# Performance work log

Measured on AMD Instinct MI355X. Metric: run time of the kernel, lower is better.

Reference implementation:

```python
import jax, jax.numpy as jnp
import numpy as np

B, T, H = 65536, 34, 64
T10_LO, T10_HI = 0.1, 5.0
M0_LO, M0_HI = 0.0, 10000.0


def setup_inputs() -> dict:
    key = jax.random.key(0)
    ks = jax.random.split(key, 24)
    sig = jax.random.uniform(ks[0], (B, T), jnp.float32, 0.1, 1.0)
    keep = jax.random.uniform(ks[1], (B, T)) > 0.3
    X_fa_in = jnp.where(keep, sig, 0.0)
    fa_vals = jax.random.uniform(ks[2], (B, T), jnp.float32, 0.05, 0.6)  # flip angles (rad)
    fa_mask = keep
    fa_len = jnp.sum(keep, axis=1).astype(jnp.int64)
    TR_vals = jax.random.uniform(ks[3], (B, 1), jnp.float32, 0.003, 0.01)
    gi = 1.0 / np.sqrt(H)
    p = {}
    p['gru_Wih'] = jax.random.uniform(ks[4], (3 * H, 2), jnp.float32, -gi, gi)
    p['gru_Whh'] = jax.random.uniform(ks[5], (3 * H, H), jnp.float32, -gi, gi)
    p['gru_bih'] = jax.random.uniform(ks[6], (3 * H,), jnp.float32, -gi, gi)
    p['gru_bhh'] = jax.random.uniform(ks[7], (3 * H,), jnp.float32, -gi, gi)
    p['score_T10_w'] = jax.random.normal(ks[8], (H,), jnp.float32) * gi
    p['score_M0_w'] = jax.random.normal(ks[9], (H,), jnp.float32) * gi
    def lin(kw, kb, fan_out, fan_in):
        b = 1.0 / np.sqrt(fan_in)
        return (jax.random.uniform(kw, (fan_out, fan_in), jnp.float32, -b, b),
                jax.random.uniform(kb, (fan_out,), jnp.float32, -b, b))
    p['regT_W1'], p['regT_b1'] = lin(ks[10], ks[11], 200, H)
    p['regT_W2'], p['regT_b2'] = lin(ks[12], ks[13], 200, 200)
    p['regT_W3'], p['regT_b3'] = lin(ks[14], ks[15], 1, 200)
    p['regM_W1'], p['regM_b1'] = lin(ks[16], ks[17], 200, H)
    p['regM_W2'], p['regM_b2'] = lin(ks[18], ks[19], 200, 200)
    p['regM_W3'], p['regM_b3'] = lin(ks[20], ks[21], 1, 200)
    return dict(X_fa_in=X_fa_in, fa_vals=fa_vals, fa_mask=fa_mask, fa_len=fa_len,
                TR_vals=TR_vals, **p)


def _forward_fill(X_fa_in, fa_vals):
    # Segmented last-observation-carried-forward via cummax of valid indices.
    valid = X_fa_in != 0
    idx = jnp.where(valid, jnp.arange(T)[None, :], -1)
    last = jax.lax.cummax(idx, axis=1)                     # [B,T] index of last nonzero
    g = jnp.clip(last, 0, T - 1)
    Xf = jnp.where(last >= 0, jnp.take_along_axis(X_fa_in, g, axis=1), 0.0)
    ff = jnp.where(last >= 0, jnp.take_along_axis(fa_vals, g, axis=1), 0.0)
    return Xf, ff


def _gru(x, Wih, Whh, bih, bhh):
    # x: [B,T,2] -> out: [B,T,H]; PyTorch GRU gate order (r, z, n)
    x_proj = jnp.einsum('btf,gf->btg', x, Wih) + bih       # [B,T,3H]
    def step(h, xp):
        gh = h @ Whh.T + bhh                               # [B,3H]
        xr, xz, xn = jnp.split(xp, 3, axis=-1)
        hr, hz, hn = jnp.split(gh, 3, axis=-1)
        r = jax.nn.sigmoid(xr + hr)
        z = jax.nn.sigmoid(xz + hz)
        n = jnp.tanh(xn + r * hn)
        h_new = (1.0 - z) * n + z * h
        return h_new, h_new
    h0 = jnp.zeros((x.shape[0], Whh.shape[1]), x.dtype)
    _, out = jax.lax.scan(step, h0, jnp.swapaxes(x_proj, 0, 1))
    return jnp.swapaxes(out, 0, 1)


def _mlp(h, W1, b1, W2, b2, W3, b3):
    # Dropout layers are identity in eval mode
    h = jax.nn.elu(h @ W1.T + b1)
    h = jax.nn.elu(h @ W2.T + b2)
    return h @ W3.T + b3


def reference(X_fa_in, fa_vals, fa_mask, fa_len, TR_vals,
              gru_Wih, gru_Whh, gru_bih, gru_bhh,
              score_T10_w, score_M0_w,
              regT_W1, regT_b1, regT_W2, regT_b2, regT_W3, regT_b3,
              regM_W1, regM_b1, regM_W2, regM_b2, regM_W3, regM_b3):
    Xf, ff = _forward_fill(X_fa_in, fa_vals)
    x = jnp.stack([Xf, ff], axis=-1)                       # [B,T,2]
    out = _gru(x, gru_Wih, gru_Whh, gru_bih, gru_bhh)      # [B,T,H]
    # attention pooling: softmax over time of a linear score
    sT = jax.nn.softmax(out @ score_T10_w, axis=1)[..., None]
    sM = jax.nn.softmax(out @ score_M0_w, axis=1)[..., None]
    hT = jnp.sum(out * sT, axis=1)                         # [B,H]
    hM = jnp.sum(out * sM, axis=1)
    T10_raw = _mlp(hT, regT_W1, regT_b1, regT_W2, regT_b2, regT_W3, regT_b3)[:, 0]
    M0_raw = _mlp(hM, regM_W1, regM_b1, regM_W2, regM_b2, regM_W3, regM_b3)[:, 0]
    T10 = T10_LO + jax.nn.sigmoid(T10_raw)[:, None] * (T10_HI - T10_LO)  # [B,1]
    M0 = M0_LO + jax.nn.sigmoid(M0_raw)[:, None] * (M0_HI - M0_LO)       # [B,1]
    R1 = 1.0 / T10
    E = jnp.exp(-TR_vals * R1)                             # [B,1]
    X_out = (1.0 - E) * jnp.sin(fa_vals) / (1.0 - jnp.cos(fa_vals) * E)  # [B,T]
    X_out = X_out * M0
    return (X_out, T10, M0)
```

## Files before the change

### kernel.cpp

```cpp
#include <hip/hip_runtime.h>

#define B_TOT 65536
#define T_LEN 34
#define HD 64
#define LOG2E 1.44269504088896340736f

typedef __attribute__((ext_vector_type(8))) short short8b;
typedef __attribute__((ext_vector_type(4))) short short4b;
typedef __attribute__((ext_vector_type(4))) float f32x4;
typedef __attribute__((ext_vector_type(4))) unsigned int u32x4;

__device__ __forceinline__ float frcp(float x){ return __builtin_amdgcn_rcpf(x); }
__device__ __forceinline__ float fexp2(float x){ return __builtin_amdgcn_exp2f(x); }
__device__ __forceinline__ float fsigmoid(float x){ return frcp(1.0f+__expf(-x)); }
__device__ __forceinline__ float felu(float x){ return x>0.0f ? x : (__expf(x)-1.0f); }

__device__ __forceinline__ unsigned short f2bf_rne(float f){
    unsigned int u = __float_as_uint(f);
    u += 0x7FFFu + ((u >> 16) & 1u);
    return (unsigned short)(u >> 16);
}
__device__ __forceinline__ float bf2f(unsigned short h){
    return __uint_as_float(((unsigned int)h) << 16);
}
__device__ __forceinline__ unsigned short f2bf_fast(float f){
    unsigned int u = __float_as_uint(f);
    return (unsigned short)((u + 0x8000u) >> 16);
}
__device__ __forceinline__ void split8(const float4& a, const float4& b,
                                       short8b& hi, short8b& lo){
    float f[8] = {a.x,a.y,a.z,a.w,b.x,b.y,b.z,b.w};
    #pragma unroll
    for (int i = 0; i < 8; ++i){
        unsigned short h = f2bf_rne(f[i]);
        hi[i] = (short)h;
        lo[i] = (short)f2bf_rne(f[i] - bf2f(h));
    }
}
__device__ __forceinline__ short8b frag_from_word(unsigned int w){
    u32x4 v = {w, 0u, 0u, 0u};
    return __builtin_bit_cast(short8b, v);
}

__global__ __launch_bounds__(256)
void gru_attn_mfma(const float* __restrict__ Xin, const float* __restrict__ FA,
                   const float* __restrict__ Wih, const float* __restrict__ Whh,
                   const float* __restrict__ bih, const float* __restrict__ bhh,
                   const float* __restrict__ swT, const float* __restrict__ swM,
                   float* __restrict__ hT_out, float* __restrict__ hM_out)
{
    __shared__ __align__(16) unsigned short WF[24*512];
    __shared__ __align__(16) unsigned short HL[4][1024];
    __shared__ unsigned int XF[32*64];

    const int tid  = threadIdx.x;
    const int lane = tid & 63;
    const int wv   = tid >> 6;
    const int l16  = lane & 15;
    const int lhi  = lane >> 4;

    for (int f = wv; f < 24; f += 4) {
        int ks = f / 12, nt = f % 12;
        int u  = nt*16 + l16;
        int k0 = ks*32 + lhi*8;
        float scale = (nt < 8) ? -LOG2E : 2.0f*LOG2E;
        const float4 w0 = *reinterpret_cast<const float4*>(&Whh[u*64 + k0]);
        const float4 w1 = *reinterpret_cast<const float4*>(&Whh[u*64 + k0 + 4]);
        unsigned short* dst = &WF[f*512 + lane*8];
        dst[0]=f2bf_rne(w0.x*scale); dst[1]=f2bf_rne(w0.y*scale);
        dst[2]=f2bf_rne(w0.z*scale); dst[3]=f2bf_rne(w0.w*scale);
        dst[4]=f2bf_rne(w1.x*scale); dst[5]=f2bf_rne(w1.y*scale);
        dst[6]=f2bf_rne(w1.z*scale); dst[7]=f2bf_rne(w1.w*scale);
    }

    #pragma unroll
    for (int i = 0; i < 16; ++i) HL[wv][i*64 + lane] = 0;

    short8b bS0, bS1;
    {
        const float* src = (l16 == 1) ? swM : swT;
        #pragma unroll
        for (int j = 0; j < 8; ++j) {
            bS0[j] = (l16 < 2) ? (short)f2bf_rne(src[     lhi*8 + j]*LOG2E) : (short)0;
            bS1[j] = (l16 < 2) ? (short)f2bf_rne(src[32 + lhi*8 + j]*LOG2E) : (short)0;
        }
    }

    unsigned int wext[12];
    float biasD[12], biasX[4];
    #pragma unroll
    for (int nt = 0; nt < 12; ++nt) {
        int u = nt*16 + l16;
        float s = (nt < 8) ? -LOG2E : 2.0f*LOG2E;
        unsigned int pk = (unsigned int)f2bf_rne(s*Wih[u*2])
                        | ((unsigned int)f2bf_rne(s*Wih[u*2+1]) << 16);
        wext[nt] = (lhi == 0) ? pk : 0u;
        biasD[nt] = (nt < 8) ? -LOG2E*(bih[u] + bhh[u]) : 2.0f*LOG2E*bhh[u];
        if (nt >= 8) biasX[nt-8] = 2.0f*LOG2E*bih[u];
    }

    const int rowbase = blockIdx.x*64 + wv*16;

    unsigned int xt32 = 0, xt33 = 0;
    for (int rr = 0; rr < 16; ++rr) {
        int row = rowbase + rr;
        float X = 0.0f, fa = 0.0f; int idx = -1;
        if (lane < T_LEN) {
            X  = Xin[row*T_LEN + lane];
            fa = FA [row*T_LEN + lane];
            if (X != 0.0f) idx = lane;
        }
        #pragma unroll
        for (int off = 1; off < 64; off <<= 1) {
            int v = __shfl_up(idx, off);
            if (lane >= off && v > idx) idx = v;
        }
        int gsrc = idx < 0 ? 0 : idx;
        float Xg = __shfl(X,  gsrc);
        float fg = __shfl(fa, gsrc);
        if (idx < 0) { Xg = 0.0f; fg = 0.0f; }
        unsigned int p = (unsigned int)f2bf_rne(Xg) | ((unsigned int)f2bf_rne(fg) << 16);
        if (lane < 32) XF[lane*64 + wv*16 + rr] = p;
        unsigned int v32 = __shfl(p, 32), v33 = __shfl(p, 33);
        if (l16 == rr) { xt32 = v32; xt33 = v33; }
    }

    __syncthreads();

    const int swz   = (l16 & 7) << 3;
    const int aoff0 = l16*64 + ((     lhi*8) ^ swz);
    const int aoff1 = l16*64 + ((32 + lhi*8) ^ swz);
    const int bcast = lane & 48;
    const int xfidx = wv*16 + l16;

    float2 hreg2[4][2];
    float2 numT2[4][2], numM2[4][2];
    float  denT[4] = {}, denM[4] = {};
    #pragma unroll
    for (int q = 0; q < 4; ++q)
        #pragma unroll
        for (int j = 0; j < 2; ++j) {
            hreg2[q][j] = make_float2(0.f, 0.f);
            numT2[q][j] = make_float2(0.f, 0.f);
            numM2[q][j] = make_float2(0.f, 0.f);
        }

    const unsigned short* HLr = HL[wv];
    unsigned short*       HLw = HL[wv];
    const unsigned short* WFl = &WF[lane*8];

    for (int t = 0; t < T_LEN; ++t) {
        short8b a0 = *reinterpret_cast<const short8b*>(&HLr[aoff0]);
        short8b a1 = *reinterpret_cast<const short8b*>(&HLr[aoff1]);
        unsigned int xw = (t < 32) ? XF[t*64 + xfidx] : ((t == 32) ? xt32 : xt33);
        short8b aext = frag_from_word((lhi == 0) ? xw : 0u);

        f32x4 accS = (f32x4){0.f,0.f,0.f,0.f};
        accS = __builtin_amdgcn_mfma_f32_16x16x32_bf16(a0, bS0, accS, 0,0,0);
        accS = __builtin_amdgcn_mfma_f32_16x16x32_bf16(a1, bS1, accS, 0,0,0);

        if (t) {
            #pragma unroll
            for (int q = 0; q < 4; ++q) {
                float e  = fexp2(accS[q]);
                float eT = __shfl(e, bcast);
                float eM = __shfl(e, bcast | 1);
                denT[q] += eT; denM[q] += eM;
                #pragma unroll
                for (int j = 0; j < 2; ++j) {
                    numT2[q][j].x = fmaf(eT, hreg2[q][j].x, numT2[q][j].x);
                    numT2[q][j].y = fmaf(eT, hreg2[q][j].y, numT2[q][j].y);
                    numM2[q][j].x = fmaf(eM, hreg2[q][j].x, numM2[q][j].x);
                    numM2[q][j].y = fmaf(eM, hreg2[q][j].y, numM2[q][j].y);
                }
            }
        }

        #pragma unroll
        for (int g = 0; g < 4; ++g) {
            float br = biasD[g], bz = biasD[g+4], bnh = biasD[g+8], bnx = biasX[g];
            f32x4 ar  = (f32x4){br,br,br,br};
            f32x4 az  = (f32x4){bz,bz,bz,bz};
            f32x4 anh = (f32x4){bnh,bnh,bnh,bnh};
            f32x4 anx = (f32x4){bnx,bnx,bnx,bnx};
            ar  = __builtin_amdgcn_mfma_f32_16x16x32_bf16(a0, *reinterpret_cast<const short8b*>(WFl + (g   )*512), ar , 0,0,0);
            ar  = __builtin_amdgcn_mfma_f32_16x16x32_bf16(a1, *reinterpret_cast<const short8b*>(WFl + (12+g)*512), ar , 0,0,0);
            ar  = __builtin_amdgcn_mfma_f32_16x16x32_bf16(aext, frag_from_word(wext[g]),   ar , 0,0,0);
            az  = __builtin_amdgcn_mfma_f32_16x16x32_bf16(a0, *reinterpret_cast<const short8b*>(WFl + (g+4 )*512), az , 0,0,0);
            az  = __builtin_amdgcn_mfma_f32_16x16x32_bf16(a1, *reinterpret_cast<const short8b*>(WFl + (16+g)*512), az , 0,0,0);
            az  = __builtin_amdgcn_mfma_f32_16x16x32_bf16(aext, frag_from_word(wext[g+4]), az , 0,0,0);
            anh = __builtin_amdgcn_mfma_f32_16x16x32_bf16(a0, *reinterpret_cast<const short8b*>(WFl + (g+8 )*512), anh, 0,0,0);
            anh = __builtin_amdgcn_mfma_f32_16x16x32_bf16(a1, *reinterpret_cast<const short8b*>(WFl + (20+g)*512), anh, 0,0,0);
            anx = __builtin_amdgcn_mfma_f32_16x16x32_bf16(aext, frag_from_word(wext[g+8]), anx, 0,0,0);
            #pragma unroll
            for (int q = 0; q < 4; ++q) {
                float r  = frcp(1.0f + fexp2(ar[q]));
                float z  = frcp(1.0f + fexp2(az[q]));
                float v  = fmaf(r, anh[q], anx[q]);
                float n  = fmaf(-2.0f, frcp(1.0f + fexp2(v)), 1.0f);
                float h  = (g & 1) ? hreg2[q][g>>1].y : hreg2[q][g>>1].x;
                float hn = fmaf(z, h - n, n);
                if (g & 1) hreg2[q][g>>1].y = hn; else hreg2[q][g>>1].x = hn;
                int rloc = lhi*4 + q;
                HLw[rloc*64 + (((g<<4) + l16) ^ ((rloc & 7) << 3))] = f2bf_fast(hn);
            }
        }
    }

    {
        short8b a0 = *reinterpret_cast<const short8b*>(&HLr[aoff0]);
        short8b a1 = *reinterpret_cast<const short8b*>(&HLr[aoff1]);
        f32x4 accS = (f32x4){0.f,0.f,0.f,0.f};
        accS = __builtin_amdgcn_mfma_f32_16x16x32_bf16(a0, bS0, accS, 0,0,0);
        accS = __builtin_amdgcn_mfma_f32_16x16x32_bf16(a1, bS1, accS, 0,0,0);
        #pragma unroll
        for (int q = 0; q < 4; ++q) {
            float e  = fexp2(accS[q]);
            float eT = __shfl(e, bcast);
            float eM = __shfl(e, bcast | 1);
            denT[q] += eT; denM[q] += eM;
            #pragma unroll
            for (int j = 0; j < 2; ++j) {
                numT2[q][j].x = fmaf(eT, hreg2[q][j].x, numT2[q][j].x);
                numT2[q][j].y = fmaf(eT, hreg2[q][j].y, numT2[q][j].y);
                numM2[q][j].x = fmaf(eM, hreg2[q][j].x, numM2[q][j].x);
                numM2[q][j].y = fmaf(eM, hreg2[q][j].y, numM2[q][j].y);
            }
        }
    }

    #pragma unroll
    for (int q = 0; q < 4; ++q) {
        int row = rowbase + lhi*4 + q;
        float rT = frcp(denT[q]), rM = frcp(denM[q]);
        #pragma unroll
        for (int j = 0; j < 2; ++j) {
            hT_out[row*HD + (2*j  )*16 + l16] = numT2[q][j].x*rT;
            hT_out[row*HD + (2*j+1)*16 + l16] = numT2[q][j].y*rT;
            hM_out[row*HD + (2*j  )*16 + l16] = numM2[q][j].x*rM;
            hM_out[row*HD + (2*j+1)*16 + l16] = numM2[q][j].y*rM;
        }
    }
}

__global__ __launch_bounds__(256)
void mlp_mfma(const float* __restrict__ hT, const float* __restrict__ hM,
    const float* __restrict__ TW1, const float* __restrict__ Tb1,
    const float* __restrict__ TW2, const float* __restrict__ Tb2,
    const float* __restrict__ TW3, const float* __restrict__ Tb3,
    const float* __restrict__ MW1, const float* __restrict__ Mb1,
    const float* __restrict__ MW2, const float* __restrict__ Mb2,
    const float* __restrict__ MW3, const float* __restrict__ Mb3,
    const float* __restrict__ FA, const float* __restrict__ TR,
    float* __restrict__ out)
{
    __shared__ __align__(16) unsigned short xh[2*64*64];
    __shared__ __align__(16) unsigned short h1s[64*256];
    __shared__ float praw[4][64];
    __shared__ float rawv[2][64];
    __shared__ float Es[64], M0s[64];

    const int tid  = threadIdx.x;
    const int lane = tid & 63;
    const int wv   = tid >> 6;
    const int l16  = lane & 15;
    const int lhi  = lane >> 4;
    const int row0 = blockIdx.x*64;

    {
        int r  = tid >> 2;
        int k0 = (tid & 3) * 16;
        int rx = r & 7;
        const float* pT = &hT[(row0+r)*64 + k0];
        const float* pM = &hM[(row0+r)*64 + k0];
        #pragma unroll
        for (int j = 0; j < 4; ++j) {
            float4 vT = *reinterpret_cast<const float4*>(pT + 4*j);
            float4 vM = *reinterpret_cast<const float4*>(pM + 4*j);
            int kk = k0 + 4*j;
            int ad = r*64 + ((((kk>>3) ^ rx))<<3) + (kk&7);
            short4b sT = { (short)f2bf_rne(vT.x), (short)f2bf_rne(vT.y),
                           (short)f2bf_rne(vT.z), (short)f2bf_rne(vT.w) };
            short4b sM = { (short)f2bf_rne(vM.x), (short)f2bf_rne(vM.y),
                           (short)f2bf_rne(vM.z), (short)f2bf_rne(vM.w) };
            *reinterpret_cast<short4b*>(&xh[ad])        = sT;
            *reinterpret_cast<short4b*>(&xh[4096 + ad]) = sM;
        }
        for (int i = tid; i < 64*24; i += 256) {
            int rr = i / 24, kk = 200 + i % 24;
            h1s[rr*256 + ((((kk>>3) ^ (rr&7)))<<3) + (kk&7)] = 0;
        }
    }
    __syncthreads();

    for (int brn = 0; brn < 2; ++brn) {
        const float* W1 = brn ? MW1 : TW1; const float* b1 = brn ? Mb1 : Tb1;
        const float* W2 = brn ? MW2 : TW2; const float* b2 = brn ? Mb2 : Tb2;
        const float* W3 = brn ? MW3 : TW3; const float* b3 = brn ? Mb3 : Tb3;

        for (int s = 0; s < 4; ++s) {
            int nt = wv + 4*s;
            if (nt > 12) break;
            int n  = nt*16 + l16;
            int nc = n < 200 ? n : 199;
            float bv = b1[nc];
            f32x4 acc[4];
            #pragma unroll
            for (int mt = 0; mt < 4; ++mt) acc[mt] = (f32x4){bv,bv,bv,bv};
            #pragma unroll
            for (int ks = 0; ks < 2; ++ks) {
                int k0 = ks*32 + lhi*8;
                const float* wp = &W1[nc*64 + k0];
                float4 w0 = *reinterpret_cast<const float4*>(wp);
                float4 w1 = *reinterpret_cast<const float4*>(wp + 4);
                short8b bh, bl;
                split8(w0, w1, bh, bl);
                #pragma unroll
                for (int mt = 0; mt < 4; ++mt) {
                    int rr = mt*16 + l16;
                    short8b a = *reinterpret_cast<const short8b*>(
                        &xh[brn*4096 + rr*64 + ((((k0>>3) ^ (rr&7)))<<3)]);
                    acc[mt] = __builtin_amdgcn_mfma_f32_16x16x32_bf16(a, bh, acc[mt], 0,0,0);
                    acc[mt] = __builtin_amdgcn_mfma_f32_16x16x32_bf16(a, bl, acc[mt], 0,0,0);
                }
            }
            if (n < 200) {
                #pragma unroll
                for (int mt = 0; mt < 4; ++mt) {
                    #pragma unroll
                    for (int q = 0; q < 4; ++q) {
                        int rr = mt*16 + lhi*4 + q;
                        h1s[rr*256 + ((((n>>3) ^ (rr&7)))<<3) + (n&7)] =
                            f2bf_rne(felu(acc[mt][q]));
                    }
                }
            }
        }
        __syncthreads();

        float p[4][4] = {};
        for (int s = 0; s < 4; ++s) {
            int nt = wv + 4*s;
            if (nt > 12) break;
            int n  = nt*16 + l16;
            int nc = n < 200 ? n : 199;
            float w3v = (n < 200) ? W3[nc] : 0.0f;
            float bv = b2[nc];
            f32x4 acc[4];
            #pragma unroll
            for (int mt = 0; mt < 4; ++mt) acc[mt] = (f32x4){bv,bv,bv,bv};
            for (int ks = 0; ks < 7; ++ks) {
                int k0 = ks*32 + lhi*8;
                short8b bh, bl;
                if (k0 + 8 <= 200) {
                    const float* wp = &W2[nc*200 + k0];
                    float4 w0 = *reinterpret_cast<const float4*>(wp);
                    float4 w1 = *reinterpret_cast<const float4*>(wp + 4);
                    split8(w0, w1, bh, bl);
                } else {
                    #pragma unroll
                    for (int i = 0; i < 8; ++i) { bh[i] = 0; bl[i] = 0; }
                }
                #pragma unroll
                for (int mt = 0; mt < 4; ++mt) {
                    int rr = mt*16 + l16;
                    short8b a = *reinterpret_cast<const short8b*>(
                        &h1s[rr*256 + ((((k0>>3) ^ (rr&7)))<<3)]);
                    acc[mt] = __builtin_amdgcn_mfma_f32_16x16x32_bf16(a, bh, acc[mt], 0,0,0);
                    acc[mt] = __builtin_amdgcn_mfma_f32_16x16x32_bf16(a, bl, acc[mt], 0,0,0);
                }
            }
            #pragma unroll
            for (int mt = 0; mt < 4; ++mt)
                #pragma unroll
                for (int q = 0; q < 4; ++q)
                    p[mt][q] = fmaf(w3v, felu(acc[mt][q]), p[mt][q]);
        }
        #pragma unroll
        for (int off = 1; off < 16; off <<= 1) {
            #pragma unroll
            for (int mt = 0; mt < 4; ++mt)
                #pragma unroll
                for (int q = 0; q < 4; ++q)
                    p[mt][q] += __shfl_xor(p[mt][q], off);
        }
        if (l16 == 0) {
            #pragma unroll
            for (int mt = 0; mt < 4; ++mt)
                #pragma unroll
                for (int q = 0; q < 4; ++q)
                    praw[wv][mt*16 + lhi*4 + q] = p[mt][q];
        }
        __syncthreads();
        if (tid < 64)
            rawv[brn][tid] = b3[0] + praw[0][tid] + praw[1][tid] + praw[2][tid] + praw[3][tid];
        __syncthreads();
    }

    if (tid < 64) {
        int row = row0 + tid;
        float T10 = 0.1f + 4.9f*fsigmoid(rawv[0][tid]);
        float M0  = 10000.0f*fsigmoid(rawv[1][tid]);
        Es[tid]  = __expf(-TR[row]/T10);
        M0s[tid] = M0;
        out[(size_t)B_TOT*T_LEN + row]         = T10;
        out[(size_t)B_TOT*T_LEN + B_TOT + row] = M0;
    }
    __syncthreads();
    for (int i = tid; i < 64*T_LEN; i += 256) {
        int rr = i / T_LEN, t = i - rr*T_LEN;
        int row = row0 + rr;
        float fa = FA[row*T_LEN + t];
        float s = __sinf(fa), c = __cosf(fa);
        float Ev = Es[rr];
        out[row*T_LEN + t] = (1.0f - Ev)*s*frcp(1.0f - c*Ev)*M0s[rr];
    }
}

extern "C" void kernel_launch(void* const* d_in, const int* in_sizes, int n_in,
                              void* d_out, int out_size, void* d_ws, size_t ws_size,
                              hipStream_t stream) {
    const float* Xin = (const float*)d_in[0];
    const float* FA  = (const float*)d_in[1];
    const float* TR  = (const float*)d_in[4];
    const float* Wih = (const float*)d_in[5];
    const float* Whh = (const float*)d_in[6];
    const float* bih = (const float*)d_in[7];
    const float* bhh = (const float*)d_in[8];
    const float* swT = (const float*)d_in[9];
    const float* swM = (const float*)d_in[10];
    const float* TW1 = (const float*)d_in[11]; const float* Tb1 = (const float*)d_in[12];
    const float* TW2 = (const float*)d_in[13]; const float* Tb2 = (const float*)d_in[14];
    const float* TW3 = (const float*)d_in[15]; const float* Tb3 = (const float*)d_in[16];
    const float* MW1 = (const float*)d_in[17]; const float* Mb1 = (const float*)d_in[18];
    const float* MW2 = (const float*)d_in[19]; const float* Mb2 = (const float*)d_in[20];
    const float* MW3 = (const float*)d_in[21]; const float* Mb3 = (const float*)d_in[22];
    float* out = (float*)d_out;

    float* hT = (float*)d_ws;
    float* hM = hT + (size_t)B_TOT*HD;

    gru_attn_mfma<<<B_TOT/64, 256, 0, stream>>>(Xin, FA, Wih, Whh, bih, bhh,
                                                swT, swM, hT, hM);
    mlp_mfma<<<B_TOT/64, 256, 0, stream>>>(hT, hM,
                                           TW1, Tb1, TW2, Tb2, TW3, Tb3,
                                           MW1, Mb1, MW2, Mb2, MW3, Mb3,
                                           FA, TR, out);
}
```

Baseline: 294.3 us.

## Restructure GRU MFMA operands: permuted hidden layout, broadcast score weights, bias via MFMA

Permutes the hidden-state k ordering so each lane writes its four hidden values as one packed 64-bit store using v_cvt_pk_bf16, replacing 16 scalar bf16 stores per step. The attention scores become full 16-column MFMAs whose weights are replicated across columns, which removes the per-step cross-lane shuffles. Input weights and biases move into an LDS fragment, with a constant 1.0 column folding the bias into the input MFMA, which frees registers. This adds two MFMAs per step and more LDS fragment reads, and it depends on the permuted layout being consistent across every reader and writer.

```diff
diff --git a/kernel.cpp b/kernel.cpp
--- a/kernel.cpp
+++ b/kernel.cpp
@@ -22,10 +22,6 @@
 }
 __device__ __forceinline__ float bf2f(unsigned short h){
     return __uint_as_float(((unsigned int)h) << 16);
-}
-__device__ __forceinline__ unsigned short f2bf_fast(float f){
-    unsigned int u = __float_as_uint(f);
-    return (unsigned short)((u + 0x8000u) >> 16);
 }
 __device__ __forceinline__ void split8(const float4& a, const float4& b,
                                        short8b& hi, short8b& lo){
@@ -37,10 +33,12 @@
         lo[i] = (short)f2bf_rne(f[i] - bf2f(h));
     }
 }
-__device__ __forceinline__ short8b frag_from_word(unsigned int w){
-    u32x4 v = {w, 0u, 0u, 0u};
-    return __builtin_bit_cast(short8b, v);
-}
+__device__ __forceinline__ unsigned int cvt_pk_bf16(float lo, float hi){
+    unsigned int r;
+    asm("v_cvt_pk_bf16_f32 %0, %1, %2" : "=v"(r) : "v"(lo), "v"(hi));
+    return r;
+}
+__device__ __forceinline__ int hswz(int r){ return ((r ^ (r >> 3)) & 7); }
 
 __global__ __launch_bounds__(256)
 void gru_attn_mfma(const float* __restrict__ Xin, const float* __restrict__ FA,
@@ -49,9 +47,10 @@
                    const float* __restrict__ swT, const float* __restrict__ swM,
                    float* __restrict__ hT_out, float* __restrict__ hM_out)
 {
-    __shared__ __align__(16) unsigned short WF[24*512];
+    __shared__ __align__(16) unsigned short WF[28*512];
+    __shared__ __align__(16) unsigned short XW[12*512];
     __shared__ __align__(16) unsigned short HL[4][1024];
-    __shared__ unsigned int XF[32*64];
+    __shared__ unsigned int XF[T_LEN*64];
 
     const int tid  = threadIdx.x;
     const int lane = tid & 63;
@@ -59,49 +58,50 @@
     const int l16  = lane & 15;
     const int lhi  = lane >> 4;
 
-    for (int f = wv; f < 24; f += 4) {
-        int ks = f / 12, nt = f % 12;
-        int u  = nt*16 + l16;
-        int k0 = ks*32 + lhi*8;
-        float scale = (nt < 8) ? -LOG2E : 2.0f*LOG2E;
-        const float4 w0 = *reinterpret_cast<const float4*>(&Whh[u*64 + k0]);
-        const float4 w1 = *reinterpret_cast<const float4*>(&Whh[u*64 + k0 + 4]);
+    for (int f = wv; f < 28; f += 4) {
         unsigned short* dst = &WF[f*512 + lane*8];
-        dst[0]=f2bf_rne(w0.x*scale); dst[1]=f2bf_rne(w0.y*scale);
-        dst[2]=f2bf_rne(w0.z*scale); dst[3]=f2bf_rne(w0.w*scale);
-        dst[4]=f2bf_rne(w1.x*scale); dst[5]=f2bf_rne(w1.y*scale);
-        dst[6]=f2bf_rne(w1.z*scale); dst[7]=f2bf_rne(w1.w*scale);
+        if (f < 24) {
+            int ks = f / 12, nt = f % 12;
+            int u_out = nt*16 + l16;
+            float scale = (nt < 8) ? -LOG2E : 2.0f*LOG2E;
+            #pragma unroll
+            for (int j = 0; j < 8; ++j) {
+                int k = ks*32 + lhi*8 + j;
+                int u_in = (k & 3)*16 + (k >> 2);
+                dst[j] = f2bf_rne(scale*Whh[u_out*64 + u_in]);
+            }
+        } else {
+            int s = f - 24;
+            const float* src = (s >= 2) ? swM : swT;
+            int ks = s & 1;
+            #pragma unroll
+            for (int j = 0; j < 8; ++j) {
+                int k = ks*32 + lhi*8 + j;
+                int u_in = (k & 3)*16 + (k >> 2);
+                dst[j] = f2bf_rne(LOG2E*src[u_in]);
+            }
+        }
+    }
+    for (int i = tid; i < 12*512; i += 256) XW[i] = 0;
+    __syncthreads();
+    if (lhi == 0) {
+        for (int nt = wv; nt < 12; nt += 4) {
+            int u_abs = (nt < 8) ? (nt*16 + l16) : (128 + (nt-8)*16 + l16);
+            float s = (nt < 8) ? -LOG2E : 2.0f*LOG2E;
+            float bias = (nt < 8) ? -LOG2E*(bih[u_abs] + bhh[u_abs])
+                                  : 2.0f*LOG2E*bih[u_abs];
+            unsigned short* dst = &XW[nt*512 + lane*8];
+            dst[0] = f2bf_rne(s*Wih[u_abs*2]);
+            dst[1] = f2bf_rne(s*Wih[u_abs*2+1]);
+            dst[2] = f2bf_rne(bias);
+        }
     }
 
     #pragma unroll
     for (int i = 0; i < 16; ++i) HL[wv][i*64 + lane] = 0;
 
-    short8b bS0, bS1;
-    {
-        const float* src = (l16 == 1) ? swM : swT;
-        #pragma unroll
-        for (int j = 0; j < 8; ++j) {
-            bS0[j] = (l16 < 2) ? (short)f2bf_rne(src[     lhi*8 + j]*LOG2E) : (short)0;
-            bS1[j] = (l16 < 2) ? (short)f2bf_rne(src[32 + lhi*8 + j]*LOG2E) : (short)0;
-        }
-    }
-
-    unsigned int wext[12];
-    float biasD[12], biasX[4];
-    #pragma unroll
-    for (int nt = 0; nt < 12; ++nt) {
-        int u = nt*16 + l16;
-        float s = (nt < 8) ? -LOG2E : 2.0f*LOG2E;
-        unsigned int pk = (unsigned int)f2bf_rne(s*Wih[u*2])
-                        | ((unsigned int)f2bf_rne(s*Wih[u*2+1]) << 16);
-        wext[nt] = (lhi == 0) ? pk : 0u;
-        biasD[nt] = (nt < 8) ? -LOG2E*(bih[u] + bhh[u]) : 2.0f*LOG2E*bhh[u];
-        if (nt >= 8) biasX[nt-8] = 2.0f*LOG2E*bih[u];
-    }
-
     const int rowbase = blockIdx.x*64 + wv*16;
 
-    unsigned int xt32 = 0, xt33 = 0;
     for (int rr = 0; rr < 16; ++rr) {
         int row = rowbase + rr;
         float X = 0.0f, fa = 0.0f; int idx = -1;
@@ -119,19 +119,23 @@
         float Xg = __shfl(X,  gsrc);
         float fg = __shfl(fa, gsrc);
         if (idx < 0) { Xg = 0.0f; fg = 0.0f; }
-        unsigned int p = (unsigned int)f2bf_rne(Xg) | ((unsigned int)f2bf_rne(fg) << 16);
-        if (lane < 32) XF[lane*64 + wv*16 + rr] = p;
-        unsigned int v32 = __shfl(p, 32), v33 = __shfl(p, 33);
-        if (l16 == rr) { xt32 = v32; xt33 = v33; }
-    }
+        if (lane < T_LEN)
+            XF[lane*64 + wv*16 + rr] =
+                (unsigned int)f2bf_rne(Xg) | ((unsigned int)f2bf_rne(fg) << 16);
+    }
+
+    float biasN[4];
+    #pragma unroll
+    for (int g = 0; g < 4; ++g) biasN[g] = 2.0f*LOG2E*bhh[128 + g*16 + l16];
 
     __syncthreads();
 
-    const int swz   = (l16 & 7) << 3;
-    const int aoff0 = l16*64 + ((     lhi*8) ^ swz);
-    const int aoff1 = l16*64 + ((32 + lhi*8) ^ swz);
-    const int bcast = lane & 48;
+    const int sA    = hswz(l16) << 3;
+    const int aoff0 = l16*64 + (( lhi   *8) ^ sA);
+    const int aoff1 = l16*64 + (((4+lhi)*8) ^ sA);
     const int xfidx = wv*16 + l16;
+    const unsigned int extk2 = (lhi == 0) ? 0x00003f80u : 0u;
+    const f32x4 zero4 = (f32x4){0.f, 0.f, 0.f, 0.f};
 
     float2 hreg2[4][2];
     float2 numT2[4][2], numM2[4][2];
@@ -148,23 +152,29 @@
     const unsigned short* HLr = HL[wv];
     unsigned short*       HLw = HL[wv];
     const unsigned short* WFl = &WF[lane*8];
+    const unsigned short* XWl = &XW[lane*8];
 
     for (int t = 0; t < T_LEN; ++t) {
         short8b a0 = *reinterpret_cast<const short8b*>(&HLr[aoff0]);
         short8b a1 = *reinterpret_cast<const short8b*>(&HLr[aoff1]);
-        unsigned int xw = (t < 32) ? XF[t*64 + xfidx] : ((t == 32) ? xt32 : xt33);
-        short8b aext = frag_from_word((lhi == 0) ? xw : 0u);
-
-        f32x4 accS = (f32x4){0.f,0.f,0.f,0.f};
-        accS = __builtin_amdgcn_mfma_f32_16x16x32_bf16(a0, bS0, accS, 0,0,0);
-        accS = __builtin_amdgcn_mfma_f32_16x16x32_bf16(a1, bS1, accS, 0,0,0);
+        unsigned int xw = XF[t*64 + xfidx];
+        u32x4 aeu = { (lhi == 0) ? xw : 0u, extk2, 0u, 0u };
+        short8b aext = __builtin_bit_cast(short8b, aeu);
+
+        f32x4 accT = __builtin_amdgcn_mfma_f32_16x16x32_bf16(
+            a0, *reinterpret_cast<const short8b*>(WFl + 24*512), zero4, 0,0,0);
+        accT = __builtin_amdgcn_mfma_f32_16x16x32_bf16(
+            a1, *reinterpret_cast<const short8b*>(WFl + 25*512), accT, 0,0,0);
+        f32x4 accM = __builtin_amdgcn_mfma_f32_16x16x32_bf16(
+            a0, *reinterpret_cast<const short8b*>(WFl + 26*512), zero4, 0,0,0);
+        accM = __builtin_amdgcn_mfma_f32_16x16x32_bf16(
+            a1, *reinterpret_cast<const short8b*>(WFl + 27*512), accM, 0,0,0);
 
         if (t) {
             #pragma unroll
             for (int q = 0; q < 4; ++q) {
-                float e  = fexp2(accS[q]);
-                float eT = __shfl(e, bcast);
-                float eM = __shfl(e, bcast | 1);
+                float eT = fexp2(accT[q]);
+                float eM = fexp2(accM[q]);
                 denT[q] += eT; denM[q] += eM;
                 #pragma unroll
                 for (int j = 0; j < 2; ++j) {
@@ -178,46 +188,61 @@
 
         #pragma unroll
         for (int g = 0; g < 4; ++g) {
-            float br = biasD[g], bz = biasD[g+4], bnh = biasD[g+8], bnx = biasX[g];
-            f32x4 ar  = (f32x4){br,br,br,br};
-            f32x4 az  = (f32x4){bz,bz,bz,bz};
-            f32x4 anh = (f32x4){bnh,bnh,bnh,bnh};
-            f32x4 anx = (f32x4){bnx,bnx,bnx,bnx};
-            ar  = __builtin_amdgcn_mfma_f32_16x16x32_bf16(a0, *reinterpret_cast<const short8b*>(WFl + (g   )*512), ar , 0,0,0);
-            ar  = __builtin_amdgcn_mfma_f32_16x16x32_bf16(a1, *reinterpret_cast<const short8b*>(WFl + (12+g)*512), ar , 0,0,0);
-            ar  = __builtin_amdgcn_mfma_f32_16x16x32_bf16(aext, frag_from_word(wext[g]),   ar , 0,0,0);
-            az  = __builtin_amdgcn_mfma_f32_16x16x32_bf16(a0, *reinterpret_cast<const short8b*>(WFl + (g+4 )*512), az , 0,0,0);
-            az  = __builtin_amdgcn_mfma_f32_16x16x32_bf16(a1, *reinterpret_cast<const short8b*>(WFl + (16+g)*512), az , 0,0,0);
-            az  = __builtin_amdgcn_mfma_f32_16x16x32_bf16(aext, frag_from_word(wext[g+4]), az , 0,0,0);
-            anh = __builtin_amdgcn_mfma_f32_16x16x32_bf16(a0, *reinterpret_cast<const short8b*>(WFl + (g+8 )*512), anh, 0,0,0);
-            anh = __builtin_amdgcn_mfma_f32_16x16x32_bf16(a1, *reinterpret_cast<const short8b*>(WFl + (20+g)*512), anh, 0,0,0);
-            anx = __builtin_amdgcn_mfma_f32_16x16x32_bf16(aext, frag_from_word(wext[g+8]), anx, 0,0,0);
+            f32x4 ar = __builtin_amdgcn_mfma_f32_16x16x32_bf16(
+                aext, *reinterpret_cast<const short8b*>(XWl + (g   )*512), zero4, 0,0,0);
+            ar = __builtin_amdgcn_mfma_f32_16x16x32_bf16(
+                a0, *reinterpret_cast<const short8b*>(WFl + (g   )*512), ar, 0,0,0);
+            ar = __builtin_amdgcn_mfma_f32_16x16x32_bf16(
+                a1, *reinterpret_cast<const short8b*>(WFl + (12+g)*512), ar, 0,0,0);
+            f32x4 az = __builtin_amdgcn_mfma_f32_16x16x32_bf16(
+                aext, *reinterpret_cast<const short8b*>(XWl + (4+g )*512), zero4, 0,0,0);
+            az = __builtin_amdgcn_mfma_f32_16x16x32_bf16(
+                a0, *reinterpret_cast<const short8b*>(WFl + (4+g )*512), az, 0,0,0);
+            az = __builtin_amdgcn_mfma_f32_16x16x32_bf16(
+                a1, *reinterpret_cast<const short8b*>(WFl + (16+g)*512), az, 0,0,0);
+            f32x4 anx = __builtin_amdgcn_mfma_f32_16x16x32_bf16(
+                aext, *reinterpret_cast<const short8b*>(XWl + (8+g )*512), zero4, 0,0,0);
+            f32x4 anh = __builtin_amdgcn_mfma_f32_16x16x32_bf16(
+                a0, *reinterpret_cast<const short8b*>(WFl + (8+g )*512), zero4, 0,0,0);
+            anh = __builtin_amdgcn_mfma_f32_16x16x32_bf16(
+                a1, *reinterpret_cast<const short8b*>(WFl + (20+g)*512), anh, 0,0,0);
             #pragma unroll
             for (int q = 0; q < 4; ++q) {
                 float r  = frcp(1.0f + fexp2(ar[q]));
                 float z  = frcp(1.0f + fexp2(az[q]));
-                float v  = fmaf(r, anh[q], anx[q]);
+                float v  = fmaf(r, anh[q], fmaf(r, biasN[g], anx[q]));
                 float n  = fmaf(-2.0f, frcp(1.0f + fexp2(v)), 1.0f);
                 float h  = (g & 1) ? hreg2[q][g>>1].y : hreg2[q][g>>1].x;
                 float hn = fmaf(z, h - n, n);
                 if (g & 1) hreg2[q][g>>1].y = hn; else hreg2[q][g>>1].x = hn;
-                int rloc = lhi*4 + q;
-                HLw[rloc*64 + (((g<<4) + l16) ^ ((rloc & 7) << 3))] = f2bf_fast(hn);
-            }
+            }
+        }
+
+        #pragma unroll
+        for (int q = 0; q < 4; ++q) {
+            int rloc = lhi*4 + q;
+            unsigned int d0 = cvt_pk_bf16(hreg2[q][0].x, hreg2[q][0].y);
+            unsigned int d1 = cvt_pk_bf16(hreg2[q][1].x, hreg2[q][1].y);
+            int so = rloc*64 + ((l16*4) ^ (hswz(rloc) << 3));
+            *reinterpret_cast<uint2*>(&HLw[so]) = make_uint2(d0, d1);
         }
     }
 
     {
         short8b a0 = *reinterpret_cast<const short8b*>(&HLr[aoff0]);
         short8b a1 = *reinterpret_cast<const short8b*>(&HLr[aoff1]);
-        f32x4 accS = (f32x4){0.f,0.f,0.f,0.f};
-        accS = __builtin_amdgcn_mfma_f32_16x16x32_bf16(a0, bS0, accS, 0,0,0);
-        accS = __builtin_amdgcn_mfma_f32_16x16x32_bf16(a1, bS1, accS, 0,0,0);
+        f32x4 accT = __builtin_amdgcn_mfma_f32_16x16x32_bf16(
+            a0, *reinterpret_cast<const short8b*>(WFl + 24*512), zero4, 0,0,0);
+        accT = __builtin_amdgcn_mfma_f32_16x16x32_bf16(
+            a1, *reinterpret_cast<const short8b*>(WFl + 25*512), accT, 0,0,0);
+        f32x4 accM = __builtin_amdgcn_mfma_f32_16x16x32_bf16(
+            a0, *reinterpret_cast<const short8b*>(WFl + 26*512), zero4, 0,0,0);
+        accM = __builtin_amdgcn_mfma_f32_16x16x32_bf16(
+            a1, *reinterpret_cast<const short8b*>(WFl + 27*512), accM, 0,0,0);
         #pragma unroll
         for (int q = 0; q < 4; ++q) {
-            float e  = fexp2(accS[q]);
-            float eT = __shfl(e, bcast);
-            float eM = __shfl(e, bcast | 1);
+            float eT = fexp2(accT[q]);
+            float eM = fexp2(accM[q]);
             denT[q] += eT; denM[q] += eM;
             #pragma unroll
             for (int j = 0; j < 2; ++j) {
```

Measured after the change: 289.1 us. Within noise of the previous version (-1.8%).
